# Kernel optimization log

Hardware: AMD Instinct MI355X
Metric: run time of the kernel (lower is better)

Reference implementation:

```python
import jax, jax.numpy as jnp
import numpy as np

NR_TRIALS = 5000
KERNEL_LEN = 201
KERNEL_STD = 30.0

# Gaussian smoothing window: signal.gaussian(201, std=30) with first 100 taps zeroed (causal half)
def _make_window():
    w = np.exp(-0.5 * ((np.arange(KERNEL_LEN) - 100) / KERNEL_STD) ** 2)
    w[:100] = 0.0
    return jnp.asarray(w, dtype=jnp.float32)

WINDOW = _make_window()


def setup_inputs() -> dict:
    key = jax.random.key(0)
    ks = jax.random.split(key, 10)
    B, N, T, H, S = 512, 8192, NR_TRIALS, 5, 10
    max_val = float(np.sqrt(1.0 / H))
    inp = {
        "x": jax.random.normal(ks[0], (B, N), dtype=jnp.float32),
        "history": jax.random.normal(ks[1], (B, N, H), dtype=jnp.float32),
        "gain": jax.random.normal(ks[2], (B,), dtype=jnp.float32),  # unused, kept for signature parity
        "state": jax.random.normal(ks[3], (B, S), dtype=jnp.float32),
        "sort_id": jax.random.randint(ks[4], (B, 1), 0, T, dtype=jnp.int64),
        "history_weights": jax.random.uniform(ks[5], (N, H), minval=-max_val, maxval=max_val, dtype=jnp.float32),
        "history_bias": jax.random.uniform(ks[6], (N,), minval=-max_val, maxval=max_val, dtype=jnp.float32),
        "state_W": jax.random.normal(ks[7], (N, S), dtype=jnp.float32) * 0.3,  # nn.Linear(S -> N) weight
        "state_b": jax.random.normal(ks[8], (N,), dtype=jnp.float32) * 0.1,
        "own_gain": jax.random.normal(ks[9], (T,), dtype=jnp.float32) * 0.1,
        "gain_adjust": jnp.ones((N,), dtype=jnp.float32),
    }
    return inp


def reference(x, history, gain, state, sort_id, history_weights, history_bias,
              state_W, state_b, own_gain, gain_adjust):
    # history modulation: einsum over the small history dim + bias
    hist = jnp.einsum("bnh,nh->bn", history, history_weights) + history_bias
    x = x + hist
    # behavioral state encoder (Linear S->N) + elu, added to x
    state_mod = state @ state_W.T + state_b
    x = x + jax.nn.elu(state_mod)
    x = jax.nn.elu(x) + 1.0
    # gain path: conv1d('same', 201-tap kernel) of a one-hot at sort_id, dotted with own_gain,
    # is exactly a windowed gather-dot: batch_gain[b] = sum_k WINDOW[k] * own_gain[sort_id[b] + 100 - k]
    T = own_gain.shape[0]
    s = sort_id[:, 0].astype(jnp.int32)                      # [B]
    idx = s[:, None] + 100 - jnp.arange(KERNEL_LEN)          # [B, 201]
    valid = (idx >= 0) & (idx < T)
    g = jnp.where(valid, own_gain[jnp.clip(idx, 0, T - 1)], 0.0)
    batch_gain = (g * WINDOW).sum(axis=-1, keepdims=True)    # [B, 1] (channel dim e=1)
    batch_gain = jax.nn.elu(batch_gain) + 1.0
    # per-neuron gain adjust
    x = (1.0 + gain_adjust[None, :] * batch_gain) * x
    return x
```

## Files before the change

kernel.cpp:

```cpp
#include <hip/hip_runtime.h>
#include <math.h>
#include <stdint.h>

#define Bsz 512
#define Nn 8192
#define Hh 5
#define Ss 10
#define KB 8
#define TILE 1024
#define NT 256
#define TILES (Nn / TILE)

#define LDS_FLOATS 15360

__device__ __forceinline__ float elu1(float v) {
    return v > 0.0f ? v : expm1f(v);
}

__device__ __forceinline__ void gload16(const float* src, float* dst) {
    __builtin_amdgcn_global_load_lds(
        (const __attribute__((address_space(1))) uint32_t*)src,
        (__attribute__((address_space(3))) uint32_t*)dst, 16, 0, 0);
}

__global__ __launch_bounds__(NT, 2) void main_kernel(
    const float* __restrict__ x,
    const float* __restrict__ history,
    const float* __restrict__ state,
    const float* __restrict__ hw,
    const float* __restrict__ hb,
    const float* __restrict__ sW,
    const float* __restrict__ sb,
    const float* __restrict__ ga,
    const int*   __restrict__ sort_id,
    const float* __restrict__ own_gain,
    float* __restrict__ out)
{
    __shared__ __align__(16) float lds[LDS_FLOATS];

    const int tid  = threadIdx.x;
    const int lane = tid & 63;
    const int wave = tid >> 6;
    const int tile  = blockIdx.x & (TILES - 1);
    const int chunk = blockIdx.x / TILES;
    const int n0 = tile * TILE;
    const int b0 = chunk * KB;
    const int nq = n0 + tid * 4;

    float* myreg = &lds[wave * 2560];
    float* myhw  = &lds[10240 + wave * 1280];

    float4 hbv = *reinterpret_cast<const float4*>(hb + nq);
    float4 sbv = *reinterpret_cast<const float4*>(sb + nq);
    float4 gav = *reinterpret_cast<const float4*>(ga + nq);

    float bgv[KB];
    {
        int grp = lane >> 3;
        int r   = lane & 7;
        int s   = sort_id[b0 + grp];
        int jmax = s < 100 ? s : 100;
        float acc = 0.0f;
        #pragma unroll
        for (int k = 0; k < 13; ++k) {
            int j = r + k * 8;
            if (j <= jmax) {
                float t = (float)j * (1.0f / 30.0f);
                acc = fmaf(expf(-0.5f * t * t), own_gain[s - j], acc);
            }
        }
        acc += __shfl_xor(acc, 1);
        acc += __shfl_xor(acc, 2);
        acc += __shfl_xor(acc, 4);
        #pragma unroll
        for (int g = 0; g < KB; ++g)
            bgv[g] = elu1(__shfl(acc, g * 8)) + 1.0f;
    }

    {
        const float* srcS = sW + (size_t)n0 * Ss + wave * 2560 + lane * 4;
        #pragma unroll
        for (int p = 0; p < 10; ++p) gload16(srcS + p * 256, myreg + p * 256);
        const float* srcA = hw + (size_t)n0 * Hh + wave * 1280 + lane * 4;
        #pragma unroll
        for (int p = 0; p < 5; ++p)  gload16(srcA + p * 256, myhw + p * 256);
    }
    asm volatile("s_waitcnt vmcnt(0)" ::: "memory");

    float wS[40], wA[20];
    #pragma unroll
    for (int i = 0; i < 10; ++i) {
        float4 t = *reinterpret_cast<float4*>(&myreg[lane * 40 + i * 4]);
        wS[i*4+0] = t.x; wS[i*4+1] = t.y; wS[i*4+2] = t.z; wS[i*4+3] = t.w;
    }
    #pragma unroll
    for (int i = 0; i < 5; ++i) {
        float4 t = *reinterpret_cast<float4*>(&myhw[lane * 20 + i * 4]);
        wA[i*4+0] = t.x; wA[i*4+1] = t.y; wA[i*4+2] = t.z; wA[i*4+3] = t.w;
    }
    asm volatile("" ::: "memory");

    {
        const float* src = history + ((size_t)b0 * Nn + n0) * Hh + wave * 1280 + lane * 4;
        #pragma unroll
        for (int p = 0; p < 5; ++p) gload16(src + p * 256, myreg + p * 256);
    }
    float4 xv = *reinterpret_cast<const float4*>(x + (size_t)b0 * Nn + nq);

    #pragma unroll
    for (int kb = 0; kb < KB; ++kb) {
        const int b = b0 + kb;

        asm volatile("s_waitcnt vmcnt(0)" ::: "memory");

        float4 xnext = xv;
        if (kb + 1 < KB) {
            const float* src = history + ((size_t)(b + 1) * Nn + n0) * Hh
                               + wave * 1280 + lane * 4;
            float* dst = myreg + ((kb + 1) & 1) * 1280;
            #pragma unroll
            for (int p = 0; p < 5; ++p) gload16(src + p * 256, dst + p * 256);
            xnext = *reinterpret_cast<const float4*>(x + (size_t)(b + 1) * Nn + nq);
        }

        float st[Ss];
        #pragma unroll
        for (int i = 0; i < Ss; ++i) st[i] = state[b * Ss + i];

        const float* buf = myreg + (kb & 1) * 1280 + lane * 20;
        float hist[4] = {hbv.x, hbv.y, hbv.z, hbv.w};
        #pragma unroll
        for (int i = 0; i < 5; ++i) {
            float4 h = *reinterpret_cast<const float4*>(buf + i * 4);
            float hv4[4] = {h.x, h.y, h.z, h.w};
            #pragma unroll
            for (int j = 0; j < 4; ++j) {
                int f = i * 4 + j;
                hist[f / Hh] = fmaf(hv4[j], wA[f], hist[f / Hh]);
            }
        }

        float sm[4] = {sbv.x, sbv.y, sbv.z, sbv.w};
        #pragma unroll
        for (int f = 0; f < 40; ++f)
            sm[f / Ss] = fmaf(st[f % Ss], wS[f], sm[f / Ss]);

        float xa[4]  = {xv.x, xv.y, xv.z, xv.w};
        float gaa[4] = {gav.x, gav.y, gav.z, gav.w};
        float res[4];
        #pragma unroll
        for (int q = 0; q < 4; ++q) {
            float v = xa[q] + hist[q] + elu1(sm[q]);
            res[q] = fmaf(gaa[q], bgv[kb], 1.0f) * (elu1(v) + 1.0f);
        }
        *reinterpret_cast<float4*>(out + (size_t)b * Nn + nq) =
            make_float4(res[0], res[1], res[2], res[3]);

        xv = xnext;
    }
}

extern "C" void kernel_launch(void* const* d_in, const int* in_sizes, int n_in,
                              void* d_out, int out_size, void* d_ws, size_t ws_size,
                              hipStream_t stream) {
    const float* x        = (const float*)d_in[0];
    const float* history  = (const float*)d_in[1];
    const float* state    = (const float*)d_in[3];
    const int*   sort_id  = (const int*)d_in[4];
    const float* hw       = (const float*)d_in[5];
    const float* hb       = (const float*)d_in[6];
    const float* sW       = (const float*)d_in[7];
    const float* sb       = (const float*)d_in[8];
    const float* own_gain = (const float*)d_in[9];
    const float* ga       = (const float*)d_in[10];
    float* out = (float*)d_out;

    const int nblocks = TILES * (Bsz / KB);
    main_kernel<<<nblocks, NT, 0, stream>>>(x, history, state, hw, hb, sW, sb,
                                            ga, sort_id, own_gain, out);
}
```

Before: 27.13 us.

## Halve batch rows per block, shrink LDS, raise occupancy and relax vmcnt waits

Each block now processes 4 batch rows instead of 8, which doubles the grid. The history-weight staging reuses the same LDS region as the state weights, cutting LDS per block so launch bounds can request 4 blocks per CU. The per-iteration wait drops from vmcnt(0) to partial counts so the prefetch of the next history tile and x overlaps the current compute. It also swaps expm1f/expf for __expf, with a small precision risk, and rebalances the gain-window reduction across 16 lanes. With fewer rows per block, the weight loads are amortised over less work, and the hand-tuned vmcnt counts depend on the compiler's exact load ordering, so a miscount could read stale LDS.

```diff
diff --git a/kernel.cpp b/kernel.cpp
--- a/kernel.cpp
+++ b/kernel.cpp
@@ -6,15 +6,15 @@
 #define Nn 8192
 #define Hh 5
 #define Ss 10
-#define KB 8
+#define KB 4
 #define TILE 1024
 #define NT 256
 #define TILES (Nn / TILE)
 
-#define LDS_FLOATS 15360
+#define LDS_FLOATS 10240
 
 __device__ __forceinline__ float elu1(float v) {
-    return v > 0.0f ? v : expm1f(v);
+    return v > 0.0f ? v : __expf(v) - 1.0f;
 }
 
 __device__ __forceinline__ void gload16(const float* src, float* dst) {
@@ -23,7 +23,7 @@
         (__attribute__((address_space(3))) uint32_t*)dst, 16, 0, 0);
 }
 
-__global__ __launch_bounds__(NT, 2) void main_kernel(
+__global__ __launch_bounds__(NT, 4) void main_kernel(
     const float* __restrict__ x,
     const float* __restrict__ history,
     const float* __restrict__ state,
@@ -48,7 +48,6 @@
     const int nq = n0 + tid * 4;
 
     float* myreg = &lds[wave * 2560];
-    float* myhw  = &lds[10240 + wave * 1280];
 
     float4 hbv = *reinterpret_cast<const float4*>(hb + nq);
     float4 sbv = *reinterpret_cast<const float4*>(sb + nq);
@@ -56,76 +55,88 @@
 
     float bgv[KB];
     {
-        int grp = lane >> 3;
-        int r   = lane & 7;
+        int grp = lane >> 4;
+        int r   = lane & 15;
         int s   = sort_id[b0 + grp];
         int jmax = s < 100 ? s : 100;
         float acc = 0.0f;
         #pragma unroll
-        for (int k = 0; k < 13; ++k) {
-            int j = r + k * 8;
+        for (int k = 0; k < 7; ++k) {
+            int j = r + k * 16;
             if (j <= jmax) {
                 float t = (float)j * (1.0f / 30.0f);
-                acc = fmaf(expf(-0.5f * t * t), own_gain[s - j], acc);
+                acc = fmaf(__expf(-0.5f * t * t), own_gain[s - j], acc);
             }
         }
         acc += __shfl_xor(acc, 1);
         acc += __shfl_xor(acc, 2);
         acc += __shfl_xor(acc, 4);
+        acc += __shfl_xor(acc, 8);
         #pragma unroll
         for (int g = 0; g < KB; ++g)
-            bgv[g] = elu1(__shfl(acc, g * 8)) + 1.0f;
+            bgv[g] = elu1(__shfl(acc, g * 16)) + 1.0f;
     }
 
     {
         const float* srcS = sW + (size_t)n0 * Ss + wave * 2560 + lane * 4;
         #pragma unroll
         for (int p = 0; p < 10; ++p) gload16(srcS + p * 256, myreg + p * 256);
-        const float* srcA = hw + (size_t)n0 * Hh + wave * 1280 + lane * 4;
-        #pragma unroll
-        for (int p = 0; p < 5; ++p)  gload16(srcA + p * 256, myhw + p * 256);
     }
     asm volatile("s_waitcnt vmcnt(0)" ::: "memory");
-
-    float wS[40], wA[20];
+    float wS[40];
     #pragma unroll
     for (int i = 0; i < 10; ++i) {
         float4 t = *reinterpret_cast<float4*>(&myreg[lane * 40 + i * 4]);
         wS[i*4+0] = t.x; wS[i*4+1] = t.y; wS[i*4+2] = t.z; wS[i*4+3] = t.w;
     }
+    asm volatile("s_waitcnt lgkmcnt(0)" ::: "memory");
+
+    {
+        const float* srcA = hw + (size_t)n0 * Hh + wave * 1280 + lane * 4;
+        #pragma unroll
+        for (int p = 0; p < 5; ++p) gload16(srcA + p * 256, myreg + p * 256);
+    }
+    asm volatile("s_waitcnt vmcnt(0)" ::: "memory");
+    float wA[20];
     #pragma unroll
     for (int i = 0; i < 5; ++i) {
-        float4 t = *reinterpret_cast<float4*>(&myhw[lane * 20 + i * 4]);
+        float4 t = *reinterpret_cast<float4*>(&myreg[lane * 20 + i * 4]);
         wA[i*4+0] = t.x; wA[i*4+1] = t.y; wA[i*4+2] = t.z; wA[i*4+3] = t.w;
     }
-    asm volatile("" ::: "memory");
+    asm volatile("s_waitcnt lgkmcnt(0)" ::: "memory");
 
     {
-        const float* src = history + ((size_t)b0 * Nn + n0) * Hh + wave * 1280 + lane * 4;
+        const float* h0 = history + ((size_t)b0 * Nn + n0) * Hh + wave * 1280 + lane * 4;
         #pragma unroll
-        for (int p = 0; p < 5; ++p) gload16(src + p * 256, myreg + p * 256);
+        for (int p = 0; p < 5; ++p) gload16(h0 + p * 256, myreg + p * 256);
     }
+    asm volatile("" ::: "memory");
     float4 xv = *reinterpret_cast<const float4*>(x + (size_t)b0 * Nn + nq);
+    asm volatile("" ::: "memory");
 
     #pragma unroll
     for (int kb = 0; kb < KB; ++kb) {
         const int b = b0 + kb;
 
-        asm volatile("s_waitcnt vmcnt(0)" ::: "memory");
-
-        float4 xnext = xv;
-        if (kb + 1 < KB) {
-            const float* src = history + ((size_t)(b + 1) * Nn + n0) * Hh
-                               + wave * 1280 + lane * 4;
-            float* dst = myreg + ((kb + 1) & 1) * 1280;
-            #pragma unroll
-            for (int p = 0; p < 5; ++p) gload16(src + p * 256, dst + p * 256);
-            xnext = *reinterpret_cast<const float4*>(x + (size_t)(b + 1) * Nn + nq);
-        }
+        if (kb == 0) asm volatile("s_waitcnt vmcnt(1)" ::: "memory");
+        else         asm volatile("s_waitcnt vmcnt(2)" ::: "memory");
 
         float st[Ss];
         #pragma unroll
         for (int i = 0; i < Ss; ++i) st[i] = state[b * Ss + i];
+        asm volatile("" ::: "memory");
+
+        float4 xnext = xv;
+        if (kb + 1 < KB) {
+            const float* hn = history + ((size_t)(b + 1) * Nn + n0) * Hh
+                              + wave * 1280 + lane * 4;
+            float* dst = myreg + ((kb + 1) & 1) * 1280;
+            #pragma unroll
+            for (int p = 0; p < 5; ++p) gload16(hn + p * 256, dst + p * 256);
+            asm volatile("" ::: "memory");
+            xnext = *reinterpret_cast<const float4*>(x + (size_t)(b + 1) * Nn + nq);
+        }
+        asm volatile("" ::: "memory");
 
         const float* buf = myreg + (kb & 1) * 1280 + lane * 20;
         float hist[4] = {hbv.x, hbv.y, hbv.z, hbv.w};
```

Result: faster. 25.68 us (-5.3%).

## Deepen history prefetch to triple buffering with smaller tiles and scalar lanes

Applied to the files above, without the earlier changes.

Halves the neuron tile to 512 per block and raises launch bounds to four blocks per CU. LDS drops to 2560 floats per wave. The weight staging buffers are reused as history buffers, giving a three-deep global_load_lds prefetch. Each lane now handles two strided scalar neurons instead of a float4, and fine-grained vmcnt waits replace the full drain. expm1f/expf are swapped for the faster __expf, which trades some accuracy for speed. The hand-counted vmcnt values must stay exactly right, and the 4-byte loads and scalar stores may lower per-instruction bandwidth.

```diff
diff --git a/kernel.cpp b/kernel.cpp
--- a/kernel.cpp
+++ b/kernel.cpp
@@ -1,20 +1,23 @@
 #include <hip/hip_runtime.h>
-#include <math.h>
 #include <stdint.h>
 
 #define Bsz 512
-#define Nn 8192
-#define Hh 5
-#define Ss 10
-#define KB 8
-#define TILE 1024
-#define NT 256
+#define Nn  8192
+#define Hh  5
+#define Ss  10
+#define KB  8
+#define TILE 512
+#define NT  256
 #define TILES (Nn / TILE)
 
-#define LDS_FLOATS 15360
+#define WREG 2560
+#define LDS_FLOATS (4 * WREG)
+
+#define FENCE() asm volatile("" ::: "memory")
+#define LGKM0() asm volatile("s_waitcnt lgkmcnt(0)" ::: "memory")
 
 __device__ __forceinline__ float elu1(float v) {
-    return v > 0.0f ? v : expm1f(v);
+    return v > 0.0f ? v : __expf(v) - 1.0f;
 }
 
 __device__ __forceinline__ void gload16(const float* src, float* dst) {
@@ -22,8 +25,20 @@
         (const __attribute__((address_space(1))) uint32_t*)src,
         (__attribute__((address_space(3))) uint32_t*)dst, 16, 0, 0);
 }
-
-__global__ __launch_bounds__(NT, 2) void main_kernel(
+__device__ __forceinline__ void gload4(const float* src, float* dst) {
+    __builtin_amdgcn_global_load_lds(
+        (const __attribute__((address_space(1))) uint32_t*)src,
+        (__attribute__((address_space(3))) uint32_t*)dst, 4, 0, 0);
+}
+
+__device__ __forceinline__ void stage640(const float* src, float* dst, int L) {
+    gload16(src + L * 4,       dst);
+    gload16(src + 256 + L * 4, dst + 256);
+    gload4 (src + 512 + L,     dst + 512);
+    gload4 (src + 576 + L,     dst + 576);
+}
+
+__global__ __launch_bounds__(NT, 4) void main_kernel(
     const float* __restrict__ x,
     const float* __restrict__ history,
     const float* __restrict__ state,
@@ -38,26 +53,26 @@
 {
     __shared__ __align__(16) float lds[LDS_FLOATS];
 
-    const int tid  = threadIdx.x;
-    const int lane = tid & 63;
-    const int wave = tid >> 6;
+    const int tid = threadIdx.x;
+    const int L   = tid & 63;
+    const int w   = tid >> 6;
     const int tile  = blockIdx.x & (TILES - 1);
     const int chunk = blockIdx.x / TILES;
     const int n0 = tile * TILE;
     const int b0 = chunk * KB;
-    const int nq = n0 + tid * 4;
-
-    float* myreg = &lds[wave * 2560];
-    float* myhw  = &lds[10240 + wave * 1280];
-
-    float4 hbv = *reinterpret_cast<const float4*>(hb + nq);
-    float4 sbv = *reinterpret_cast<const float4*>(sb + nq);
-    float4 gav = *reinterpret_cast<const float4*>(ga + nq);
-
-    float bgv[KB];
+    const int nA = n0 + 128 * w + L;
+    const int nB = nA + 64;
+    const int nwave = n0 + 128 * w;
+
+    float* WB  = &lds[w * WREG];
+    float* RsW = WB;
+    float* Rhw = WB + 1280;
+    float* Rb0 = WB + 1920;
+
+    float bg[KB];
     {
-        int grp = lane >> 3;
-        int r   = lane & 7;
+        int grp = L >> 3;
+        int r   = L & 7;
         int s   = sort_id[b0 + grp];
         int jmax = s < 100 ? s : 100;
         float acc = 0.0f;
@@ -66,7 +81,7 @@
             int j = r + k * 8;
             if (j <= jmax) {
                 float t = (float)j * (1.0f / 30.0f);
-                acc = fmaf(expf(-0.5f * t * t), own_gain[s - j], acc);
+                acc = fmaf(__expf(-0.5f * t * t), own_gain[s - j], acc);
             }
         }
         acc += __shfl_xor(acc, 1);
@@ -74,89 +89,107 @@
         acc += __shfl_xor(acc, 4);
         #pragma unroll
         for (int g = 0; g < KB; ++g)
-            bgv[g] = elu1(__shfl(acc, g * 8)) + 1.0f;
-    }
+            bg[g] = elu1(__shfl(acc, g * 8)) + 1.0f;
+    }
+    float hbA = hb[nA], hbB = hb[nB];
+    float sbA = sb[nA], sbB = sb[nB];
+    float gaA = ga[nA], gaB = ga[nB];
+    FENCE();
 
     {
-        const float* srcS = sW + (size_t)n0 * Ss + wave * 2560 + lane * 4;
-        #pragma unroll
-        for (int p = 0; p < 10; ++p) gload16(srcS + p * 256, myreg + p * 256);
-        const float* srcA = hw + (size_t)n0 * Hh + wave * 1280 + lane * 4;
-        #pragma unroll
-        for (int p = 0; p < 5; ++p)  gload16(srcA + p * 256, myhw + p * 256);
-    }
-    asm volatile("s_waitcnt vmcnt(0)" ::: "memory");
-
-    float wS[40], wA[20];
+        const float* s0 = sW + (size_t)nwave * Ss;
+        gload16(s0 + L * 4,        RsW);
+        gload16(s0 + 256  + L * 4, RsW + 256);
+        gload16(s0 + 512  + L * 4, RsW + 512);
+        gload16(s0 + 768  + L * 4, RsW + 768);
+        gload16(s0 + 1024 + L * 4, RsW + 1024);
+    }
+    FENCE();
+    stage640(hw + (size_t)nwave * Hh, Rhw, L);
+    FENCE();
+    stage640(history + ((size_t)b0 * Nn + nwave) * Hh, Rb0, L);
+    FENCE();
+    float xAv[KB], xBv[KB];
+    xAv[0] = x[(size_t)b0 * Nn + nA];
+    xBv[0] = x[(size_t)b0 * Nn + nB];
+    FENCE();
+
+    asm volatile("s_waitcnt vmcnt(10)" ::: "memory");
+    float wSA[10], wSB[10];
     #pragma unroll
     for (int i = 0; i < 10; ++i) {
-        float4 t = *reinterpret_cast<float4*>(&myreg[lane * 40 + i * 4]);
-        wS[i*4+0] = t.x; wS[i*4+1] = t.y; wS[i*4+2] = t.z; wS[i*4+3] = t.w;
-    }
+        wSA[i] = RsW[10 * L + i];
+        wSB[i] = RsW[640 + 10 * L + i];
+    }
+    LGKM0();
+    stage640(history + ((size_t)(b0 + 1) * Nn + nwave) * Hh, RsW, L);
+    xAv[1] = x[(size_t)(b0 + 1) * Nn + nA];
+    xBv[1] = x[(size_t)(b0 + 1) * Nn + nB];
+    FENCE();
+
+    asm volatile("s_waitcnt vmcnt(12)" ::: "memory");
+    float wAA[5], wAB[5];
     #pragma unroll
     for (int i = 0; i < 5; ++i) {
-        float4 t = *reinterpret_cast<float4*>(&myhw[lane * 20 + i * 4]);
-        wA[i*4+0] = t.x; wA[i*4+1] = t.y; wA[i*4+2] = t.z; wA[i*4+3] = t.w;
-    }
-    asm volatile("" ::: "memory");
-
-    {
-        const float* src = history + ((size_t)b0 * Nn + n0) * Hh + wave * 1280 + lane * 4;
-        #pragma unroll
-        for (int p = 0; p < 5; ++p) gload16(src + p * 256, myreg + p * 256);
-    }
-    float4 xv = *reinterpret_cast<const float4*>(x + (size_t)b0 * Nn + nq);
+        wAA[i] = Rhw[5 * L + i];
+        wAB[i] = Rhw[320 + 5 * L + i];
+    }
+    LGKM0();
+    stage640(history + ((size_t)(b0 + 2) * Nn + nwave) * Hh, Rhw, L);
+    xAv[2] = x[(size_t)(b0 + 2) * Nn + nA];
+    xBv[2] = x[(size_t)(b0 + 2) * Nn + nB];
+    FENCE();
 
     #pragma unroll
     for (int kb = 0; kb < KB; ++kb) {
+        if      (kb == 0) asm volatile("s_waitcnt vmcnt(14)" ::: "memory");
+        else if (kb == 1) asm volatile("s_waitcnt vmcnt(16)" ::: "memory");
+        else if (kb == 2) asm volatile("s_waitcnt vmcnt(18)" ::: "memory");
+        else if (kb <= 5) asm volatile("s_waitcnt vmcnt(20)" ::: "memory");
+        else if (kb == 6) asm volatile("s_waitcnt vmcnt(14)" ::: "memory");
+        else              asm volatile("s_waitcnt vmcnt(8)"  ::: "memory");
+
+        float* buf = (kb % 3 == 0) ? Rb0 : (kb % 3 == 1) ? RsW : Rhw;
         const int b = b0 + kb;
 
-        asm volatile("s_waitcnt vmcnt(0)" ::: "memory");
-
-        float4 xnext = xv;
-        if (kb + 1 < KB) {
-            const float* src = history + ((size_t)(b + 1) * Nn + n0) * Hh
-                               + wave * 1280 + lane * 4;
-            float* dst = myreg + ((kb + 1) & 1) * 1280;
-            #pragma unroll
-            for (int p = 0; p < 5; ++p) gload16(src + p * 256, dst + p * 256);
-            xnext = *reinterpret_cast<const float4*>(x + (size_t)(b + 1) * Nn + nq);
-        }
-
         float st[Ss];
         #pragma unroll
-        for (int i = 0; i < Ss; ++i) st[i] = state[b * Ss + i];
-
-        const float* buf = myreg + (kb & 1) * 1280 + lane * 20;
-        float hist[4] = {hbv.x, hbv.y, hbv.z, hbv.w};
+        for (int i = 0; i < Ss; ++i) st[i] = state[(size_t)b * Ss + i];
+
+        float hvA[5], hvB[5];
         #pragma unroll
         for (int i = 0; i < 5; ++i) {
-            float4 h = *reinterpret_cast<const float4*>(buf + i * 4);
-            float hv4[4] = {h.x, h.y, h.z, h.w};
-            #pragma unroll
-            for (int j = 0; j < 4; ++j) {
-                int f = i * 4 + j;
-                hist[f / Hh] = fmaf(hv4[j], wA[f], hist[f / Hh]);
-            }
-        }
-
-        float sm[4] = {sbv.x, sbv.y, sbv.z, sbv.w};
-        #pragma unroll
-        for (int f = 0; f < 40; ++f)
-            sm[f / Ss] = fmaf(st[f % Ss], wS[f], sm[f / Ss]);
-
-        float xa[4]  = {xv.x, xv.y, xv.z, xv.w};
-        float gaa[4] = {gav.x, gav.y, gav.z, gav.w};
-        float res[4];
-        #pragma unroll
-        for (int q = 0; q < 4; ++q) {
-            float v = xa[q] + hist[q] + elu1(sm[q]);
-            res[q] = fmaf(gaa[q], bgv[kb], 1.0f) * (elu1(v) + 1.0f);
-        }
-        *reinterpret_cast<float4*>(out + (size_t)b * Nn + nq) =
-            make_float4(res[0], res[1], res[2], res[3]);
-
-        xv = xnext;
+            hvA[i] = buf[5 * L + i];
+            hvB[i] = buf[320 + 5 * L + i];
+        }
+
+        float histA = hbA, histB = hbB;
+        #pragma unroll
+        for (int i = 0; i < 5; ++i) {
+            histA = fmaf(hvA[i], wAA[i], histA);
+            histB = fmaf(hvB[i], wAB[i], histB);
+        }
+        float smA = sbA, smB = sbB;
+        #pragma unroll
+        for (int i = 0; i < 10; ++i) {
+            smA = fmaf(st[i], wSA[i], smA);
+            smB = fmaf(st[i], wSB[i], smB);
+        }
+        float vA = xAv[kb] + histA + elu1(smA);
+        float vB = xBv[kb] + histB + elu1(smB);
+        float resA = fmaf(gaA, bg[kb], 1.0f) * (elu1(vA) + 1.0f);
+        float resB = fmaf(gaB, bg[kb], 1.0f) * (elu1(vB) + 1.0f);
+
+        LGKM0();
+        if (kb + 3 < KB) {
+            stage640(history + ((size_t)(b + 3) * Nn + nwave) * Hh, buf, L);
+            xAv[kb + 3] = x[(size_t)(b + 3) * Nn + nA];
+            xBv[kb + 3] = x[(size_t)(b + 3) * Nn + nB];
+        }
+        FENCE();
+        out[(size_t)b * Nn + nA] = resA;
+        out[(size_t)b * Nn + nB] = resB;
+        FENCE();
     }
 }
 
```

Result: faster. 25.59 us (-5.7%).
